# Kernel optimization log

Measured on AMD Instinct MI355X. Metric: run time of the kernel, lower is better.

The kernel has to match this reference:

```python
import jax, jax.numpy as jnp
import numpy as np

D_STATE = 16
LOW_RANK = 6


def _scan_fwd(t):
    # 'interwave' scan: (B, stream, signal, C, H, W) -> (stream, B, C, H*W*signal)
    st, B, C = t.shape[1], t.shape[0], t.shape[3]
    t = jnp.transpose(t, (1, 0, 3, 4, 5, 2))  # stream,B,C,H,W,signal
    return t.reshape(st, B, C, -1)


def _scan_bwd(t, sg, H, W):
    # inverse 'interwave': (stream, B, C, H*W*sg) -> (B, stream, sg, C, H, W)
    st, B, C, _ = t.shape
    t = t.reshape(st, B, C, H, W, sg)
    return jnp.transpose(t, (1, 0, 5, 2, 3, 4))


def _layernorm(t, w, b):
    # LayerNorm over last (channel) axis, eps=1e-5 (torch default)
    mu = t.mean(-1, keepdims=True)
    var = t.var(-1, keepdims=True)
    return (t - mu) * jax.lax.rsqrt(var + 1e-5) * w + b


def reference(x, x_proj_weight, dt_projs_weight, dt_projs_bias, A_logs, Ds, norm_weight, norm_bias):
    B, S, C, H, W = x.shape
    stream = S + 1
    G = 4 * stream            # scan_direction * stream groups
    N = D_STATE
    R = LOW_RANK
    L = S * H * W             # unistream_length
    i = jnp.arange(S - 1)
    j = jnp.arange(S)

    # ---- CommDiffSS2DScan (cross-scan) ----
    x_comm_0 = _scan_fwd(x[:, None])                                  # (1,B,C,L)
    x_comm_1 = _scan_fwd(jnp.swapaxes(x, -1, -2)[:, None])
    x_dif = x[:, :, None] - x[:, None, :]                             # (B,S,S,C,H,W)
    x_dif = x_dif.at[:, i, i].set(x_dif[:, i, S - 1])
    x_dif = x_dif.at[:, :, S - 1].set(x)
    x_diff_0 = _scan_fwd(x_dif)                                       # (S,B,C,L)
    x_diff_1 = _scan_fwd(jnp.swapaxes(x_dif, -1, -2))
    xs0 = jnp.concatenate([x_diff_0, x_comm_0], 0)                    # (stream,B,C,L)
    xs1 = jnp.concatenate([x_diff_1, x_comm_1], 0)
    xs = jnp.stack([xs0, xs1, xs0[..., ::-1], xs1[..., ::-1]], 0)     # (4,stream,B,C,L)
    xs = jnp.transpose(xs, (2, 0, 1, 3, 4))                           # (B,4,stream,C,L)

    # ---- input-dependent projections ----
    x_dbl = jnp.einsum('bkscl,kspc->bkspl', xs, x_proj_weight)        # (B,4,stream,R+2N,L)
    dts, Bs, Cs = jnp.split(x_dbl, [R, R + N], axis=3)
    dts = jnp.einsum('bksrl,kscr->bkscl', dts, dt_projs_weight)       # (B,4,stream,C,L)

    u = xs.reshape(B, G, C, L)
    delta = jax.nn.softplus(dts.reshape(B, G, C, L) + dt_projs_bias.reshape(G, C)[None, :, :, None])
    A = -jnp.exp(A_logs).reshape(G, C, N)
    Bm = Bs.reshape(B, G, N, L)
    Cm = Cs.reshape(B, G, N, L)

    # ---- selective scan along L ----
    def step(h, inp):
        u_, d_, b_, c_ = inp                                          # (B,G,C),(B,G,C),(B,G,N),(B,G,N)
        h = h * jnp.exp(d_[..., None] * A) + (d_ * u_)[..., None] * b_[:, :, None, :]
        return h, jnp.einsum('bgcn,bgn->bgc', h, c_)

    h0 = jnp.zeros((B, G, C, N), x.dtype)
    _, ys = jax.lax.scan(step, h0, (jnp.moveaxis(u, -1, 0), jnp.moveaxis(delta, -1, 0),
                                    jnp.moveaxis(Bm, -1, 0), jnp.moveaxis(Cm, -1, 0)))
    ys = jnp.moveaxis(ys, 0, -1) + Ds.reshape(G, C)[None, :, :, None] * u  # (B,G,C,L)

    # ---- CommDiffSS2DMerge (cross-merge) ----
    ys = jnp.transpose(ys.reshape(B, 4, stream, C, L), (1, 2, 0, 3, 4))   # (4,stream,B,C,L)
    ys = ys[:2] + ys[2:, ..., ::-1]                                       # (2,stream,B,C,L)
    yd = _scan_bwd(ys[0, :S], S, H, W) + jnp.swapaxes(_scan_bwd(ys[1, :S], S, W, H), -1, -2)
    y = yd[:, :, S - 1]
    yd = yd.at[:, i, S - 1].set(yd[:, i, i])
    yd = yd.at[:, j, j].set(0.0)
    y_dif_extend = yd.sum(2)
    y_com = (_scan_bwd(ys[0, S:], S, H, W) + jnp.swapaxes(_scan_bwd(ys[1, S:], S, W, H), -1, -2)).reshape(B, S, C, H, W)

    tocl = lambda t: jnp.transpose(t, (0, 1, 3, 4, 2))  # channels-last for out_norm
    return (_layernorm(tocl(y), norm_weight, norm_bias),
            _layernorm(tocl(y_com), norm_weight, norm_bias),
            _layernorm(tocl(y_dif_extend), norm_weight, norm_bias))


def setup_inputs() -> dict:
    key = jax.random.key(0)
    ks = jax.random.split(key, 6)
    B, S, C, H, W = 4, 2, 96, 32, 32
    stream = S + 1
    G = 4 * stream
    N, R = D_STATE, LOW_RANK
    P = N + N + R
    return {
        'x': jax.random.normal(ks[0], (B, S, C, H, W), jnp.float32),
        'x_proj_weight': jax.random.normal(ks[1], (4, stream, P, C), jnp.float32) * 0.1,
        'dt_projs_weight': jax.random.normal(ks[2], (4, stream, C, R), jnp.float32) * 0.1,
        'dt_projs_bias': jax.random.uniform(ks[3], (G * C,), jnp.float32) * 0.1,
        'A_logs': jax.random.uniform(ks[4], (G * C, N), jnp.float32),
        'Ds': jax.random.normal(ks[5], (G * C,), jnp.float32) * 0.1,
        'norm_weight': jnp.ones((C,), jnp.float32),
        'norm_bias': jnp.zeros((C,), jnp.float32),
    }
```

## Files before the change

### kernel.cpp

```cpp
#include <hip/hip_runtime.h>
#include <math.h>

typedef float f4 __attribute__((ext_vector_type(4)));
typedef float f2 __attribute__((ext_vector_type(2)));

#define L_LEN 2048
#define C_DIM 96
#define N_DIM 16
#define R_DIM 6
#define G_DIM 12
#define B_DIM 4
#define NCHUNK 64
#define CLEN 32
#define WINL 128
#define BGC (B_DIM * G_DIM * C_DIM)

#define SZ_DELTA (B_DIM * G_DIM * L_LEN * C_DIM)
#define SZ_BC (B_DIM * G_DIM * N_DIM * L_LEN)
#define SZ_U6 (B_DIM * 6 * C_DIM * L_LEN)
#define SZ_Y (B_DIM * G_DIM * C_DIM * L_LEN)
#define SZ_H (BGC * NCHUNK * N_DIM)
#define SZ_S (BGC * NCHUNK)
#define SZ_X (B_DIM * 2 * C_DIM * 1024)
#define SZ_WPAD (G_DIM * 40 * C_DIM)

__device__ __forceinline__ float fexp2(float x) { return __builtin_amdgcn_exp2f(x); }
__device__ __forceinline__ f2 pkfma(f2 a, f2 b, f2 c) { return __builtin_elementwise_fma(a, b, c); }

__device__ __forceinline__ float softplus_f(float x)
{
    float sp = __logf(1.f + __expf(x));
    return (x > 20.f) ? x : sp;
}

__global__ __launch_bounds__(256) void k0_xT(
    const float* __restrict__ x, float* __restrict__ xT)
{
    __shared__ float t[32][33];
    int img = blockIdx.x;
    const float* src = x + (size_t)img * 1024;
    float* dst = xT + (size_t)img * 1024;
    int tx = threadIdx.x & 31, ty = threadIdx.x >> 5;
#pragma unroll
    for (int r = 0; r < 32; r += 8) t[ty + r][tx] = src[(ty + r) * 32 + tx];
    __syncthreads();
#pragma unroll
    for (int r = 0; r < 32; r += 8) dst[(ty + r) * 32 + tx] = t[tx][ty + r];
}

__global__ __launch_bounds__(256) void k0b_padw(
    const float* __restrict__ xpw, float* __restrict__ wpad)
{
    int i = blockIdx.x * 256 + (int)threadIdx.x;
    if (i >= G_DIM * 40 * C_DIM) return;
    int g = i / (40 * C_DIM);
    int rem = i - g * 40 * C_DIM;
    int p = rem / C_DIM, c = rem - (rem / C_DIM) * C_DIM;
    wpad[i] = (p < 38) ? xpw[((size_t)g * 38 + p) * C_DIM + c] : 0.f;
}

__global__ __launch_bounds__(256) void k1_proj(
    const float* __restrict__ x, const float* __restrict__ xT,
    const float* __restrict__ wpad, const float* __restrict__ dtw,
    const float* __restrict__ dtb,
    float* __restrict__ deltaT, float* __restrict__ Bsw,
    float* __restrict__ Csw, float* __restrict__ u6T)
{
    __shared__ float Vsh[C_DIM * 68];
    __shared__ float Psh[40][68];

    int blk = blockIdx.x;
    int ltile = blk & 31;
    int bks = blk >> 5;
    int s = bks % 3;
    int k = (bks / 3) & 1;
    int b = bks / 6;
    int g = k * 3 + s;
    int gh = g + 6;
    int l0 = ltile * 64;
    int l0h = (31 - ltile) * 64;
    int bg = b * G_DIM + g;
    int bgh = b * G_DIM + gh;
    int tid = (int)threadIdx.x;

    const float* xb = (k ? xT : x) + (size_t)b * 2 * C_DIM * 1024;

#pragma unroll
    for (int j = 0; j < 6; ++j) {
        int e = tid + j * 256;
        int c = e >> 4;
        int llq = (e & 15) * 4;
        int pp = (l0 + llq) >> 1;
        f2 x0 = *(const f2*)(xb + (size_t)c * 1024 + pp);
        f2 x1 = *(const f2*)(xb + (size_t)(C_DIM + c) * 1024 + pp);
        f4 v;
        if (s == 2)      { v[0] = x0.x; v[1] = x1.x; v[2] = x0.y; v[3] = x1.y; }
        else if (s == 1) { v[0] = x1.x - x0.x; v[1] = x1.x; v[2] = x1.y - x0.y; v[3] = x1.y; }
        else             { v[0] = x0.x - x1.x; v[1] = x0.x; v[2] = x0.y - x1.y; v[3] = x0.y; }
        *(f4*)(Vsh + c * 68 + llq) = v;
    }
    __syncthreads();

    {
        size_t ub = ((size_t)(b * 6 + g) * L_LEN + l0) * C_DIM;
#pragma unroll
        for (int j = 0; j < 6; ++j) {
            int e = tid + j * 256;
            int lidx = e / 24;
            int c4 = (e - lidx * 24) * 4;
            f4 v = { Vsh[(c4 + 0) * 68 + lidx], Vsh[(c4 + 1) * 68 + lidx],
                     Vsh[(c4 + 2) * 68 + lidx], Vsh[(c4 + 3) * 68 + lidx] };
            *(f4*)(u6T + ub + (size_t)lidx * C_DIM + c4) = v;
        }
    }

    int ll = tid & 63;
    int P0 = __builtin_amdgcn_readfirstlane((tid >> 6) * 10);
    const float* wp = wpad + (size_t)g * 3840 + (size_t)P0 * C_DIM;
    const float* wph = wpad + (size_t)gh * 3840 + (size_t)P0 * C_DIM;

    float acc[10], acch[10];
#pragma unroll
    for (int p = 0; p < 10; ++p) { acc[p] = 0.f; acch[p] = 0.f; }

    for (int cb = 0; cb < C_DIM; cb += 8) {
        float vc[8], vch[8];
#pragma unroll
        for (int i = 0; i < 8; ++i) {
            vc[i] = Vsh[(cb + i) * 68 + ll];
            vch[i] = Vsh[(cb + i) * 68 + 63 - ll];
        }
#pragma unroll
        for (int p = 0; p < 10; ++p) {
#pragma unroll
            for (int q = 0; q < 2; ++q) {
                f4 w = *(const f4*)(wp + p * C_DIM + cb + q * 4);
                f4 wh = *(const f4*)(wph + p * C_DIM + cb + q * 4);
#pragma unroll
                for (int i = 0; i < 4; ++i) {
                    acc[p] = fmaf(w[i], vc[q * 4 + i], acc[p]);
                    acch[p] = fmaf(wh[i], vch[q * 4 + i], acch[p]);
                }
            }
        }
    }

#pragma unroll
    for (int gg = 0; gg < 2; ++gg) {
        __syncthreads();
#pragma unroll
        for (int p = 0; p < 10; ++p) Psh[P0 + p][ll] = gg ? acch[p] : acc[p];
        __syncthreads();
        int lb = gg ? l0h : l0;
        int bgx = gg ? bgh : bg;
        int gx = gg ? gh : g;
        int q = tid & 3, lx = tid >> 2;
        f4 bv = { Psh[6 + q * 4 + 0][lx], Psh[6 + q * 4 + 1][lx],
                  Psh[6 + q * 4 + 2][lx], Psh[6 + q * 4 + 3][lx] };
        *(f4*)(Bsw + ((size_t)bgx * L_LEN + lb + lx) * N_DIM + q * 4) = bv;
        f4 cv = { Psh[22 + q * 4 + 0][lx], Psh[22 + q * 4 + 1][lx],
                  Psh[22 + q * 4 + 2][lx], Psh[22 + q * 4 + 3][lx] };
        *(f4*)(Csw + ((size_t)bgx * L_LEN + lb + lx) * N_DIM + q * 4) = cv;

        const float* wdg = dtw + (size_t)gx * C_DIM * R_DIM;
        const float* biasg = dtb + gx * C_DIM;
        size_t db = ((size_t)bgx * L_LEN + lb) * C_DIM;
        for (int e = tid; e < 64 * C_DIM; e += 256) {
            int lidx = e / 96, c = e - (e / 96) * 96;
            float dsum = biasg[c];
#pragma unroll
            for (int r = 0; r < R_DIM; ++r) dsum = fmaf(Psh[r][lidx], wdg[c * R_DIM + r], dsum);
            deltaT[db + (size_t)lidx * C_DIM + c] = softplus_f(dsum);
        }
    }
}

__global__ __launch_bounds__(192) void k2_scanA(
    const float* __restrict__ deltaT, const float* __restrict__ Bsw,
    const float* __restrict__ u6T, const float* __restrict__ A_logs,
    float* __restrict__ hend, float* __restrict__ Sbuf)
{
    __shared__ f4 Bsh[512];
    int blk = blockIdx.x;
    int win = blk & 15;
    int bg = blk >> 4;
    int g = bg % G_DIM;
    int b = bg / G_DIM;
    int tid = (int)threadIdx.x;

    const f4* Bg = (const f4*)(Bsw + ((size_t)bg * L_LEN + win * WINL) * N_DIM);
    for (int i = tid; i < 512; i += 192) Bsh[i] = Bg[i];
    __syncthreads();

    int chl = tid / 48;
    int cp = tid % 48;
    int c0 = cp * 2;
    int ch = win * 4 + chl;
    const bool rev = (g >= 6);
    int gu = rev ? (g - 6) : g;

    f2 a2[N_DIM];
    {
        const f4* A0 = (const f4*)(A_logs + ((size_t)g * C_DIM + c0) * N_DIM);
        const f4* A1 = (const f4*)(A_logs + ((size_t)g * C_DIM + c0 + 1) * N_DIM);
#pragma unroll
        for (int q = 0; q < 4; ++q) {
            f4 v0 = A0[q], v1 = A1[q];
#pragma unroll
            for (int i = 0; i < 4; ++i)
                a2[q * 4 + i] = (f2){ -__expf(v0[i]) * 1.44269504f, -__expf(v1[i]) * 1.44269504f };
        }
    }

    const int LOFF = ch * CLEN;
    const float* dp = deltaT + ((size_t)bg * L_LEN + LOFF) * C_DIM + c0;
    const float* up;
    int us;
    if (rev) { up = u6T + ((size_t)(b * 6 + gu) * L_LEN + (2047 - LOFF)) * C_DIM + c0; us = -C_DIM; }
    else     { up = u6T + ((size_t)(b * 6 + gu) * L_LEN + LOFF) * C_DIM + c0; us = C_DIM; }

    f2 h2[N_DIM];
#pragma unroll
    for (int n = 0; n < N_DIM; ++n) h2[n] = (f2){0.f, 0.f};
    f2 S2 = {0.f, 0.f};

    f2 dbuf[2], ubuf[2];
#pragma unroll
    for (int j = 0; j < 2; ++j) { dbuf[j] = *(const f2*)(dp + j * C_DIM); ubuf[j] = *(const f2*)(up + j * us); }

    for (int jj = 0; jj < CLEN; jj += 2) {
        int nx = (jj + 2 < CLEN) ? jj + 2 : jj;
        f2 dn[2], un[2];
#pragma unroll
        for (int j = 0; j < 2; ++j) { dn[j] = *(const f2*)(dp + (nx + j) * C_DIM); un[j] = *(const f2*)(up + (nx + j) * us); }
#pragma unroll
        for (int j = 0; j < 2; ++j) {
            int li = chl * CLEN + jj + j;
            f2 dv = dbuf[j];
            S2 += dv;
            f2 du2 = dv * ubuf[j];
            const f4* Bl = Bsh + (size_t)li * 4;
#pragma unroll
            for (int q = 0; q < 4; ++q) {
                f4 Bq = Bl[q];
#pragma unroll
                for (int i = 0; i < 4; ++i) {
                    int n = q * 4 + i;
                    f2 m = dv * a2[n];
                    f2 e = { fexp2(m.x), fexp2(m.y) };
                    h2[n] = pkfma(h2[n], e, du2 * (f2){Bq[i], Bq[i]});
                }
            }
        }
#pragma unroll
        for (int j = 0; j < 2; ++j) { dbuf[j] = dn[j]; ubuf[j] = un[j]; }
    }
    size_t base0 = ((size_t)(bg * C_DIM + c0) * NCHUNK + ch) * N_DIM;
    size_t base1 = base0 + (size_t)NCHUNK * N_DIM;
#pragma unroll
    for (int q = 0; q < 4; ++q) {
        f4 h0 = { h2[q * 4].x, h2[q * 4 + 1].x, h2[q * 4 + 2].x, h2[q * 4 + 3].x };
        f4 h1 = { h2[q * 4].y, h2[q * 4 + 1].y, h2[q * 4 + 2].y, h2[q * 4 + 3].y };
        *(f4*)(hend + base0 + q * 4) = h0;
        *(f4*)(hend + base1 + q * 4) = h1;
    }
    Sbuf[(size_t)(bg * C_DIM + c0) * NCHUNK + ch] = S2.x;
    Sbuf[(size_t)(bg * C_DIM + c0 + 1) * NCHUNK + ch] = S2.y;
}

__global__ __launch_bounds__(256) void k2_fix(
    const float* __restrict__ Sbuf, const float* __restrict__ A_logs, float* hh)
{
    int t = blockIdx.x * 256 + (int)threadIdx.x;
    int n = t & 15;
    int bgc = t >> 4;
    int c = bgc % C_DIM;
    int g = (bgc / C_DIM) % G_DIM;
    float a2 = -__expf(A_logs[((size_t)g * C_DIM + c) * N_DIM + n]) * 1.44269504f;
    const float* Sp = Sbuf + (size_t)bgc * NCHUNK;
    float h = 0.f;
    for (int ch = 0; ch < NCHUNK; ++ch) {
        size_t idx = ((size_t)bgc * NCHUNK + ch) * N_DIM + n;
        float he = hh[idx];
        float P = fexp2(a2 * Sp[ch]);
        hh[idx] = h;
        h = fmaf(h, P, he);
    }
}

__global__ __launch_bounds__(192) void k2_scanC(
    const float* __restrict__ deltaT, const float* __restrict__ Bsw,
    const float* __restrict__ Csw, const float* __restrict__ u6T,
    const float* __restrict__ A_logs, const float* __restrict__ Ds,
    const float* __restrict__ hstart, float* __restrict__ yssT)
{
    __shared__ f4 Bsh[512];
    __shared__ f4 Csh[512];
    int blk = blockIdx.x;
    int win = blk & 15;
    int bg = blk >> 4;
    int g = bg % G_DIM;
    int b = bg / G_DIM;
    int tid = (int)threadIdx.x;

    const f4* Bg = (const f4*)(Bsw + ((size_t)bg * L_LEN + win * WINL) * N_DIM);
    const f4* Cg = (const f4*)(Csw + ((size_t)bg * L_LEN + win * WINL) * N_DIM);
    for (int i = tid; i < 512; i += 192) { Bsh[i] = Bg[i]; Csh[i] = Cg[i]; }
    __syncthreads();

    int chl = tid / 48;
    int cp = tid % 48;
    int c0 = cp * 2;
    int ch = win * 4 + chl;
    const bool rev = (g >= 6);
    int gu = rev ? (g - 6) : g;

    f2 a2[N_DIM];
    {
        const f4* A0 = (const f4*)(A_logs + ((size_t)g * C_DIM + c0) * N_DIM);
        const f4* A1 = (const f4*)(A_logs + ((size_t)g * C_DIM + c0 + 1) * N_DIM);
#pragma unroll
        for (int q = 0; q < 4; ++q) {
            f4 v0 = A0[q], v1 = A1[q];
#pragma unroll
            for (int i = 0; i < 4; ++i)
                a2[q * 4 + i] = (f2){ -__expf(v0[i]) * 1.44269504f, -__expf(v1[i]) * 1.44269504f };
        }
    }
    f2 dsc = *(const f2*)(Ds + g * C_DIM + c0);

    const int LOFF = ch * CLEN;
    const float* dp = deltaT + ((size_t)bg * L_LEN + LOFF) * C_DIM + c0;
    const float* up;
    int us;
    if (rev) { up = u6T + ((size_t)(b * 6 + gu) * L_LEN + (2047 - LOFF)) * C_DIM + c0; us = -C_DIM; }
    else     { up = u6T + ((size_t)(b * 6 + gu) * L_LEN + LOFF) * C_DIM + c0; us = C_DIM; }
    float* yp = yssT + ((size_t)bg * L_LEN + LOFF) * C_DIM + c0;

    f2 h2[N_DIM];
    {
        size_t base0 = ((size_t)(bg * C_DIM + c0) * NCHUNK + ch) * N_DIM;
        size_t base1 = base0 + (size_t)NCHUNK * N_DIM;
#pragma unroll
        for (int q = 0; q < 4; ++q) {
            f4 h0 = *(const f4*)(hstart + base0 + q * 4);
            f4 h1 = *(const f4*)(hstart + base1 + q * 4);
#pragma unroll
            for (int i = 0; i < 4; ++i) h2[q * 4 + i] = (f2){ h0[i], h1[i] };
        }
    }

    f2 dbuf[2], ubuf[2];
#pragma unroll
    for (int j = 0; j < 2; ++j) { dbuf[j] = *(const f2*)(dp + j * C_DIM); ubuf[j] = *(const f2*)(up + j * us); }

    for (int jj = 0; jj < CLEN; jj += 2) {
        int nx = (jj + 2 < CLEN) ? jj + 2 : jj;
        f2 dn[2], un[2];
#pragma unroll
        for (int j = 0; j < 2; ++j) { dn[j] = *(const f2*)(dp + (nx + j) * C_DIM); un[j] = *(const f2*)(up + (nx + j) * us); }
#pragma unroll
        for (int j = 0; j < 2; ++j) {
            int li = chl * CLEN + jj + j;
            f2 dv = dbuf[j];
            f2 uv = ubuf[j];
            f2 du2 = dv * uv;
            const f4* Bl = Bsh + (size_t)li * 4;
            const f4* Cl = Csh + (size_t)li * 4;
            f2 ya = dsc * uv, yb = {0.f, 0.f}, yc = {0.f, 0.f}, yd = {0.f, 0.f};
#pragma unroll
            for (int q = 0; q < 4; ++q) {
                f4 Bq = Bl[q];
                f4 Cq = Cl[q];
                {
                    f2 m = dv * a2[q * 4 + 0];
                    f2 e = { fexp2(m.x), fexp2(m.y) };
                    h2[q * 4 + 0] = pkfma(h2[q * 4 + 0], e, du2 * (f2){Bq[0], Bq[0]});
                    ya = pkfma(h2[q * 4 + 0], (f2){Cq[0], Cq[0]}, ya);
                }
                {
                    f2 m = dv * a2[q * 4 + 1];
                    f2 e = { fexp2(m.x), fexp2(m.y) };
                    h2[q * 4 + 1] = pkfma(h2[q * 4 + 1], e, du2 * (f2){Bq[1], Bq[1]});
                    yb = pkfma(h2[q * 4 + 1], (f2){Cq[1], Cq[1]}, yb);
                }
                {
                    f2 m = dv * a2[q * 4 + 2];
                    f2 e = { fexp2(m.x), fexp2(m.y) };
                    h2[q * 4 + 2] = pkfma(h2[q * 4 + 2], e, du2 * (f2){Bq[2], Bq[2]});
                    yc = pkfma(h2[q * 4 + 2], (f2){Cq[2], Cq[2]}, yc);
                }
                {
                    f2 m = dv * a2[q * 4 + 3];
                    f2 e = { fexp2(m.x), fexp2(m.y) };
                    h2[q * 4 + 3] = pkfma(h2[q * 4 + 3], e, du2 * (f2){Bq[3], Bq[3]});
                    yd = pkfma(h2[q * 4 + 3], (f2){Cq[3], Cq[3]}, yd);
                }
            }
            f2 yv = (ya + yb) + (yc + yd);
            *(f2*)(yp + (jj + j) * C_DIM) = yv;
        }
#pragma unroll
        for (int j = 0; j < 2; ++j) { dbuf[j] = dn[j]; ubuf[j] = un[j]; }
    }
}

__global__ __launch_bounds__(256) void k3_out(
    const float* __restrict__ yssT, const float* __restrict__ nw,
    const float* __restrict__ nb, float* __restrict__ out)
{
    __shared__ float tA[32][97];
    __shared__ float tB[32][97];
    __shared__ float ps[4][8][32];
    __shared__ float stat[4][32];

    int blk = blockIdx.x;
    int h = blk & 31;
    int bs = blk >> 5;
    int so = bs & 1;
    int b = bs >> 1;
    int tid = (int)threadIdx.x;

    auto Y = [&](int g) { return yssT + (size_t)(b * 12 + g) * L_LEN * C_DIM; };
    const float* Y0 = Y(so);
    const float* Y0r = Y(6 + so);
    const float* Y1 = Y(3 + so);
    const float* Y1r = Y(9 + so);

#pragma unroll 2
    for (int it = 0; it < 24; ++it) {
        int idx = tid + it * 256;
        int c = idx % 96, rest = idx / 96;
        int w = rest >> 1, par = rest & 1;
        int a0 = h * 64 + rest;
        int a1 = w * 64 + 2 * h + par;
        float v = Y0[(size_t)a0 * C_DIM + c] + Y0r[(size_t)(2047 - a0) * C_DIM + c]
                + Y1[(size_t)a1 * C_DIM + c] + Y1r[(size_t)(2047 - a1) * C_DIM + c];
        if (par) tA[w][c] = v; else tB[w][c] = v;
    }
    __syncthreads();

    int w = tid & 31, cg = tid >> 5;
    float sA = 0, qA = 0, sB = 0, qB = 0;
#pragma unroll
    for (int j = 0; j < 12; ++j) {
        float yv = tA[w][cg * 12 + j], dv = tB[w][cg * 12 + j];
        sA += yv; qA += yv * yv; sB += dv; qB += dv * dv;
    }
    ps[0][cg][w] = sA; ps[1][cg][w] = qA; ps[2][cg][w] = sB; ps[3][cg][w] = qB;
    __syncthreads();
    if (tid < 32) {
        int ww = tid;
        float t0 = 0, t1 = 0, t2 = 0, t3 = 0;
#pragma unroll
        for (int q = 0; q < 8; ++q) {
            t0 += ps[0][q][ww]; t1 += ps[1][q][ww];
            t2 += ps[2][q][ww]; t3 += ps[3][q][ww];
        }
        float muA = t0 * (1.f / 96.f), eqA = t1 * (1.f / 96.f);
        float muB = t2 * (1.f / 96.f), eqB = t3 * (1.f / 96.f);
        stat[0][ww] = muA; stat[1][ww] = rsqrtf(eqA - muA * muA + 1e-5f);
        stat[2][ww] = muB; stat[3][ww] = rsqrtf(eqB - muB * muB + 1e-5f);
    }
    __syncthreads();
    size_t obase = (size_t)blk * 3072;
    for (int e = tid; e < 3072; e += 256) {
        int ww = e / 96, c = e % 96;
        float wc = nw[c], bc = nb[c];
        out[obase + e] = (tA[ww][c] - stat[0][ww]) * stat[1][ww] * wc + bc;
        out[2 * 786432 + obase + e] = (tB[ww][c] - stat[2][ww]) * stat[3][ww] * wc + bc;
    }
    __syncthreads();

    const float* Y2 = Y(2);
    const float* Y2r = Y(8);
    const float* Y3 = Y(5);
    const float* Y3r = Y(11);
#pragma unroll 2
    for (int it = 0; it < 12; ++it) {
        int idx = tid + it * 256;
        int c = idx % 96, w2 = idx / 96;
        int a0 = h * 64 + 2 * w2 + so;
        int a1 = w2 * 64 + 2 * h + so;
        float v = Y2[(size_t)a0 * C_DIM + c] + Y2r[(size_t)(2047 - a0) * C_DIM + c]
                + Y3[(size_t)a1 * C_DIM + c] + Y3r[(size_t)(2047 - a1) * C_DIM + c];
        tA[w2][c] = v;
    }
    __syncthreads();
    float sC = 0, qC = 0;
#pragma unroll
    for (int j = 0; j < 12; ++j) {
        float v = tA[w][cg * 12 + j];
        sC += v; qC += v * v;
    }
    ps[0][cg][w] = sC; ps[1][cg][w] = qC;
    __syncthreads();
    if (tid < 32) {
        int ww = tid;
        float t0 = 0, t1 = 0;
#pragma unroll
        for (int q = 0; q < 8; ++q) { t0 += ps[0][q][ww]; t1 += ps[1][q][ww]; }
        float mu = t0 * (1.f / 96.f), eq = t1 * (1.f / 96.f);
        stat[0][ww] = mu; stat[1][ww] = rsqrtf(eq - mu * mu + 1e-5f);
    }
    __syncthreads();
    for (int e = tid; e < 3072; e += 256) {
        int ww = e / 96, c = e % 96;
        out[786432 + obase + e] = (tA[ww][c] - stat[0][ww]) * stat[1][ww] * nw[c] + nb[c];
    }
}

extern "C" void kernel_launch(void* const* d_in, const int* in_sizes, int n_in,
                              void* d_out, int out_size, void* d_ws, size_t ws_size,
                              hipStream_t stream)
{
    const float* x = (const float*)d_in[0];
    const float* xpw = (const float*)d_in[1];
    const float* dtw = (const float*)d_in[2];
    const float* dtb = (const float*)d_in[3];
    const float* A_logs = (const float*)d_in[4];
    const float* Ds = (const float*)d_in[5];
    const float* nw = (const float*)d_in[6];
    const float* nb = (const float*)d_in[7];
    float* out = (float*)d_out;

    float* ws = (float*)d_ws;
    float* deltaT = ws;
    float* Bsw = deltaT + SZ_DELTA;
    float* Csw = Bsw + SZ_BC;
    float* u6T = Csw + SZ_BC;
    float* yssT = u6T + SZ_U6;
    float* xT = yssT;
    float* wpad = yssT + SZ_X;
    float* hend = yssT + SZ_Y;
    float* Sbuf = hend + SZ_H;

    k0_xT<<<dim3(768), dim3(256), 0, stream>>>(x, xT);
    k0b_padw<<<dim3(180), dim3(256), 0, stream>>>(xpw, wpad);
    k1_proj<<<dim3(24 * 32), dim3(256), 0, stream>>>(x, xT, wpad, dtw, dtb, deltaT, Bsw, Csw, u6T);
    k2_scanA<<<dim3(48 * 16), dim3(192), 0, stream>>>(deltaT, Bsw, u6T, A_logs, hend, Sbuf);
    k2_fix<<<dim3(288), dim3(256), 0, stream>>>(Sbuf, A_logs, hend);
    k2_scanC<<<dim3(48 * 16), dim3(192), 0, stream>>>(deltaT, Bsw, Csw, u6T, A_logs, Ds, hend, yssT);
    k3_out<<<dim3(256), dim3(256), 0, stream>>>(yssT, nw, nb, out);
}
```

Baseline: 158.2 us.

## Split delta computation into separate kernel and halve scan block sizes

The dt low-rank projection plus softplus moves out of the projection kernel into a new k1b_delta kernel. The projection kernel now writes a small padded 8-wide dts buffer, which the new kernel reads to compute deltaT with more blocks. The scan kernels now use 96-thread blocks covering two chunks each, which doubles the block count to improve occupancy and spread across CUs. This adds one kernel launch and an extra global round trip for the dts values.

```diff
diff --git a/kernel.cpp b/kernel.cpp
--- a/kernel.cpp
+++ b/kernel.cpp
@@ -12,17 +12,16 @@
 #define B_DIM 4
 #define NCHUNK 64
 #define CLEN 32
-#define WINL 128
 #define BGC (B_DIM * G_DIM * C_DIM)
 
 #define SZ_DELTA (B_DIM * G_DIM * L_LEN * C_DIM)
+#define SZ_DTS8 (B_DIM * G_DIM * L_LEN * 8)
 #define SZ_BC (B_DIM * G_DIM * N_DIM * L_LEN)
 #define SZ_U6 (B_DIM * 6 * C_DIM * L_LEN)
 #define SZ_Y (B_DIM * G_DIM * C_DIM * L_LEN)
 #define SZ_H (BGC * NCHUNK * N_DIM)
 #define SZ_S (BGC * NCHUNK)
 #define SZ_X (B_DIM * 2 * C_DIM * 1024)
-#define SZ_WPAD (G_DIM * 40 * C_DIM)
 
 __device__ __forceinline__ float fexp2(float x) { return __builtin_amdgcn_exp2f(x); }
 __device__ __forceinline__ f2 pkfma(f2 a, f2 b, f2 c) { return __builtin_elementwise_fma(a, b, c); }
@@ -61,9 +60,8 @@
 
 __global__ __launch_bounds__(256) void k1_proj(
     const float* __restrict__ x, const float* __restrict__ xT,
-    const float* __restrict__ wpad, const float* __restrict__ dtw,
-    const float* __restrict__ dtb,
-    float* __restrict__ deltaT, float* __restrict__ Bsw,
+    const float* __restrict__ wpad,
+    float* __restrict__ dts8, float* __restrict__ Bsw,
     float* __restrict__ Csw, float* __restrict__ u6T)
 {
     __shared__ float Vsh[C_DIM * 68];
@@ -153,7 +151,6 @@
         __syncthreads();
         int lb = gg ? l0h : l0;
         int bgx = gg ? bgh : bg;
-        int gx = gg ? gh : g;
         int q = tid & 3, lx = tid >> 2;
         f4 bv = { Psh[6 + q * 4 + 0][lx], Psh[6 + q * 4 + 1][lx],
                   Psh[6 + q * 4 + 2][lx], Psh[6 + q * 4 + 3][lx] };
@@ -161,41 +158,66 @@
         f4 cv = { Psh[22 + q * 4 + 0][lx], Psh[22 + q * 4 + 1][lx],
                   Psh[22 + q * 4 + 2][lx], Psh[22 + q * 4 + 3][lx] };
         *(f4*)(Csw + ((size_t)bgx * L_LEN + lb + lx) * N_DIM + q * 4) = cv;
-
-        const float* wdg = dtw + (size_t)gx * C_DIM * R_DIM;
-        const float* biasg = dtb + gx * C_DIM;
-        size_t db = ((size_t)bgx * L_LEN + lb) * C_DIM;
-        for (int e = tid; e < 64 * C_DIM; e += 256) {
-            int lidx = e / 96, c = e - (e / 96) * 96;
-            float dsum = biasg[c];
-#pragma unroll
-            for (int r = 0; r < R_DIM; ++r) dsum = fmaf(Psh[r][lidx], wdg[c * R_DIM + r], dsum);
-            deltaT[db + (size_t)lidx * C_DIM + c] = softplus_f(dsum);
-        }
-    }
-}
-
-__global__ __launch_bounds__(192) void k2_scanA(
+#pragma unroll
+        for (int e = tid; e < 64 * 8; e += 256) {
+            int lx2 = e >> 3, r = e & 7;
+            dts8[((size_t)bgx * L_LEN + lb + lx2) * 8 + r] = (r < 6) ? Psh[r][lx2] : 0.f;
+        }
+    }
+}
+
+__global__ __launch_bounds__(256) void k1b_delta(
+    const float* __restrict__ dts8, const float* __restrict__ dtw,
+    const float* __restrict__ dtb, float* __restrict__ deltaT)
+{
+    __shared__ float Dsh[64 * 8];
+    int blk = blockIdx.x;
+    int ltile = blk & 31;
+    int bg = blk >> 5;
+    int g = bg % G_DIM;
+    int l0 = ltile * 64;
+    int tid = (int)threadIdx.x;
+
+    const f4* Dg = (const f4*)(dts8 + ((size_t)bg * L_LEN + l0) * 8);
+    if (tid < 128) ((f4*)Dsh)[tid] = Dg[tid];
+    __syncthreads();
+
+    const float* wdg = dtw + (size_t)g * C_DIM * R_DIM;
+    const float* biasg = dtb + g * C_DIM;
+    size_t db = ((size_t)bg * L_LEN + l0) * C_DIM;
+#pragma unroll
+    for (int it = 0; it < 24; ++it) {
+        int e = tid + it * 256;
+        int lidx = e / 96, c = e - (e / 96) * 96;
+        const float* wrow = wdg + c * R_DIM;
+        float dsum = biasg[c];
+#pragma unroll
+        for (int r = 0; r < R_DIM; ++r) dsum = fmaf(Dsh[lidx * 8 + r], wrow[r], dsum);
+        deltaT[db + (size_t)lidx * C_DIM + c] = softplus_f(dsum);
+    }
+}
+
+__global__ __launch_bounds__(96) void k2_scanA(
     const float* __restrict__ deltaT, const float* __restrict__ Bsw,
     const float* __restrict__ u6T, const float* __restrict__ A_logs,
     float* __restrict__ hend, float* __restrict__ Sbuf)
 {
-    __shared__ f4 Bsh[512];
+    __shared__ f4 Bsh[256];
     int blk = blockIdx.x;
-    int win = blk & 15;
-    int bg = blk >> 4;
+    int chgrp = blk & 31;
+    int bg = blk >> 5;
     int g = bg % G_DIM;
     int b = bg / G_DIM;
     int tid = (int)threadIdx.x;
 
-    const f4* Bg = (const f4*)(Bsw + ((size_t)bg * L_LEN + win * WINL) * N_DIM);
-    for (int i = tid; i < 512; i += 192) Bsh[i] = Bg[i];
+    const f4* Bg = (const f4*)(Bsw + ((size_t)bg * L_LEN + chgrp * 64) * N_DIM);
+    for (int i = tid; i < 256; i += 96) Bsh[i] = Bg[i];
     __syncthreads();
 
     int chl = tid / 48;
     int cp = tid % 48;
     int c0 = cp * 2;
-    int ch = win * 4 + chl;
+    int ch = chgrp * 2 + chl;
     const bool rev = (g >= 6);
     int gu = rev ? (g - 6) : g;
 
@@ -288,30 +310,30 @@
     }
 }
 
-__global__ __launch_bounds__(192) void k2_scanC(
+__global__ __launch_bounds__(96) void k2_scanC(
     const float* __restrict__ deltaT, const float* __restrict__ Bsw,
     const float* __restrict__ Csw, const float* __restrict__ u6T,
     const float* __restrict__ A_logs, const float* __restrict__ Ds,
     const float* __restrict__ hstart, float* __restrict__ yssT)
 {
-    __shared__ f4 Bsh[512];
-    __shared__ f4 Csh[512];
+    __shared__ f4 Bsh[256];
+    __shared__ f4 Csh[256];
     int blk = blockIdx.x;
-    int win = blk & 15;
-    int bg = blk >> 4;
+    int chgrp = blk & 31;
+    int bg = blk >> 5;
     int g = bg % G_DIM;
     int b = bg / G_DIM;
     int tid = (int)threadIdx.x;
 
-    const f4* Bg = (const f4*)(Bsw + ((size_t)bg * L_LEN + win * WINL) * N_DIM);
-    const f4* Cg = (const f4*)(Csw + ((size_t)bg * L_LEN + win * WINL) * N_DIM);
-    for (int i = tid; i < 512; i += 192) { Bsh[i] = Bg[i]; Csh[i] = Cg[i]; }
+    const f4* Bg = (const f4*)(Bsw + ((size_t)bg * L_LEN + chgrp * 64) * N_DIM);
+    const f4* Cg = (const f4*)(Csw + ((size_t)bg * L_LEN + chgrp * 64) * N_DIM);
+    for (int i = tid; i < 256; i += 96) { Bsh[i] = Bg[i]; Csh[i] = Cg[i]; }
     __syncthreads();
 
     int chl = tid / 48;
     int cp = tid % 48;
     int c0 = cp * 2;
-    int ch = win * 4 + chl;
+    int ch = chgrp * 2 + chl;
     const bool rev = (g >= 6);
     int gu = rev ? (g - 6) : g;
 
@@ -526,7 +548,8 @@
 
     float* ws = (float*)d_ws;
     float* deltaT = ws;
-    float* Bsw = deltaT + SZ_DELTA;
+    float* dts8 = deltaT + SZ_DELTA;
+    float* Bsw = dts8 + SZ_DTS8;
     float* Csw = Bsw + SZ_BC;
     float* u6T = Csw + SZ_BC;
     float* yssT = u6T + SZ_U6;
@@ -537,9 +560,10 @@
 
     k0_xT<<<dim3(768), dim3(256), 0, stream>>>(x, xT);
     k0b_padw<<<dim3(180), dim3(256), 0, stream>>>(xpw, wpad);
-    k1_proj<<<dim3(24 * 32), dim3(256), 0, stream>>>(x, xT, wpad, dtw, dtb, deltaT, Bsw, Csw, u6T);
-    k2_scanA<<<dim3(48 * 16), dim3(192), 0, stream>>>(deltaT, Bsw, u6T, A_logs, hend, Sbuf);
+    k1_proj<<<dim3(24 * 32), dim3(256), 0, stream>>>(x, xT, wpad, dts8, Bsw, Csw, u6T);
+    k1b_delta<<<dim3(48 * 32), dim3(256), 0, stream>>>(dts8, dtw, dtb, deltaT);
+    k2_scanA<<<dim3(48 * 32), dim3(96), 0, stream>>>(deltaT, Bsw, u6T, A_logs, hend, Sbuf);
     k2_fix<<<dim3(288), dim3(256), 0, stream>>>(Sbuf, A_logs, hend);
-    k2_scanC<<<dim3(48 * 16), dim3(192), 0, stream>>>(deltaT, Bsw, Csw, u6T, A_logs, Ds, hend, yssT);
+    k2_scanC<<<dim3(48 * 32), dim3(96), 0, stream>>>(deltaT, Bsw, Csw, u6T, A_logs, Ds, hend, yssT);
     k3_out<<<dim3(256), dim3(256), 0, stream>>>(yssT, nw, nb, out);
 }
```

New measurement: 174.5 us. +10.3%, slower.
